# Kernel tuning notes

Hardware: AMD Instinct MI355X
Metric: run time of the kernel (lower is better)

The kernel has to match this reference:

```python
import jax, jax.numpy as jnp
import numpy as np

NEG_SLOPE = 0.2

def gat_conv(x, src, dst, W, a_src, a_dst, b, n_nodes):
    # x: [N, Fin] -> h: [N, Fout]; edges (src->dst) incl. self-loops
    h = x @ W                                   # [N, Fout]
    as_ = h @ a_src                             # [N] per-node source score
    ad_ = h @ a_dst                             # [N] per-node dest score
    e = jax.nn.leaky_relu(as_[src] + ad_[dst], NEG_SLOPE)   # [E]
    # segment softmax over edges sharing the same destination
    e_max = jax.ops.segment_max(e, dst, num_segments=n_nodes)
    e_exp = jnp.exp(e - e_max[dst])
    e_sum = jax.ops.segment_sum(e_exp, dst, num_segments=n_nodes)
    alpha = e_exp / (e_sum[dst] + 1e-16)        # [E]
    out = jax.ops.segment_sum(alpha[:, None] * h[src], dst, num_segments=n_nodes)
    return out + b

def setup_inputs() -> dict:
    key = jax.random.key(0)
    ks = jax.random.split(key, 12)
    N, E, Fin, H = 100000, 3200000, 128, 32
    def g(k, shape, scale):
        return jax.random.normal(k, shape, dtype=jnp.float32) * scale
    return {
        "x": g(ks[0], (N, Fin), 1.0),
        "edge_index": jax.random.randint(ks[1], (2, E), 0, N, dtype=jnp.int32),
        "W1": g(ks[2], (Fin, H), 1.0 / np.sqrt(Fin)),
        "att_src1": g(ks[3], (H,), 1.0 / np.sqrt(H)),
        "att_dst1": g(ks[4], (H,), 1.0 / np.sqrt(H)),
        "b1": jnp.zeros((H,), jnp.float32),
        "W2": g(ks[5], (H, H), 1.0 / np.sqrt(H)),
        "att_src2": g(ks[6], (H,), 1.0 / np.sqrt(H)),
        "att_dst2": g(ks[7], (H,), 1.0 / np.sqrt(H)),
        "b2": jnp.zeros((H,), jnp.float32),
        "Wf": g(ks[8], (H, H), 1.0 / np.sqrt(H)),
        "bf": jnp.zeros((H,), jnp.float32),
    }

def reference(x, edge_index, W1, att_src1, att_dst1, b1, W2, att_src2, att_dst2, b2, Wf, bf):
    n_nodes = x.shape[0]
    loops = jnp.arange(n_nodes, dtype=edge_index.dtype)
    src = jnp.concatenate([edge_index[0], loops])  # add_self_loops=True (PyG default)
    dst = jnp.concatenate([edge_index[1], loops])
    h = jax.nn.relu(gat_conv(x, src, dst, W1, att_src1, att_dst1, b1, n_nodes))
    h = jax.nn.relu(gat_conv(h, src, dst, W2, att_src2, att_dst2, b2, n_nodes))
    return h @ Wf + bf
```

## Files before the change

### kernel.cpp

```cpp
#include <hip/hip_runtime.h>

#define NEG_SLOPE 0.2f
#define BK_SH 8
#define BK_SZ 256
#define MAXBUCK 512
#define EPB 8192

typedef _Float16 half8 __attribute__((ext_vector_type(8)));
typedef float f32x4 __attribute__((ext_vector_type(4)));

__global__ __launch_bounds__(256) void k_castx(const float* __restrict__ x,
                                               _Float16* __restrict__ xh,
                                               int n8) {
  int i = blockIdx.x * 256 + threadIdx.x;
  if (i >= n8) return;
  const float4* p = reinterpret_cast<const float4*>(x) + 2 * (size_t)i;
  float4 v0 = p[0], v1 = p[1];
  half8 h;
  h[0] = (_Float16)v0.x; h[1] = (_Float16)v0.y;
  h[2] = (_Float16)v0.z; h[3] = (_Float16)v0.w;
  h[4] = (_Float16)v1.x; h[5] = (_Float16)v1.y;
  h[6] = (_Float16)v1.z; h[7] = (_Float16)v1.w;
  *(reinterpret_cast<half8*>(xh) + i) = h;
}

__global__ __launch_bounds__(256) void k_castW(const float* __restrict__ W,
                                               _Float16* __restrict__ Wt) {
  for (int i = threadIdx.x; i < 128 * 32; i += 256) {
    int k = i >> 5, f = i & 31;
    Wt[f * 128 + k] = (_Float16)W[i];
  }
}

__global__ __launch_bounds__(256) void k_feat_mfma(
    const _Float16* __restrict__ xh, const _Float16* __restrict__ Wt,
    const float* __restrict__ a_src, const float* __restrict__ a_dst,
    _Float16* __restrict__ Hh, float* __restrict__ as_, float* __restrict__ ad_,
    int N) {
  int w = threadIdx.x >> 6;
  int lane = threadIdx.x & 63;
  int base = (blockIdx.x * 4 + w) * 16;
  if (base >= N) return;
  int row16 = lane & 15;
  int kg = lane >> 4;
  f32x4 acc0 = {0.f, 0.f, 0.f, 0.f};
  f32x4 acc1 = {0.f, 0.f, 0.f, 0.f};
  const half8* xa =
      reinterpret_cast<const half8*>(xh + (size_t)(base + row16) * 128 + kg * 8);
#pragma unroll
  for (int kt = 0; kt < 4; ++kt) {
    half8 a = xa[kt * 4];
    half8 b0 = *reinterpret_cast<const half8*>(Wt + (size_t)row16 * 128 +
                                               kt * 32 + kg * 8);
    half8 b1 = *reinterpret_cast<const half8*>(Wt + (size_t)(16 + row16) * 128 +
                                               kt * 32 + kg * 8);
    acc0 = __builtin_amdgcn_mfma_f32_16x16x32_f16(a, b0, acc0, 0, 0, 0);
    acc1 = __builtin_amdgcn_mfma_f32_16x16x32_f16(a, b1, acc1, 0, 0, 0);
  }
  float aS0 = a_src[row16], aS1 = a_src[16 + row16];
  float aD0 = a_dst[row16], aD1 = a_dst[16 + row16];
  float tS[4], tD[4];
#pragma unroll
  for (int r = 0; r < 4; ++r) {
    int row = base + kg * 4 + r;
    Hh[(size_t)row * 32 + row16] = (_Float16)acc0[r];
    Hh[(size_t)row * 32 + 16 + row16] = (_Float16)acc1[r];
    tS[r] = acc0[r] * aS0 + acc1[r] * aS1;
    tD[r] = acc0[r] * aD0 + acc1[r] * aD1;
  }
#pragma unroll
  for (int off = 1; off <= 8; off <<= 1) {
#pragma unroll
    for (int r = 0; r < 4; ++r) {
      tS[r] += __shfl_xor(tS[r], off, 64);
      tD[r] += __shfl_xor(tD[r], off, 64);
    }
  }
  if (row16 == 0) {
#pragma unroll
    for (int r = 0; r < 4; ++r) {
      as_[base + kg * 4 + r] = tS[r];
      ad_[base + kg * 4 + r] = tD[r];
    }
  }
}

__global__ __launch_bounds__(256) void k_feat32(
    const float* __restrict__ X, const float* __restrict__ W,
    const float* __restrict__ a_src, const float* __restrict__ a_dst,
    _Float16* __restrict__ Hh, float* __restrict__ as_, float* __restrict__ ad_,
    int N) {
  __shared__ float sW[32 * 32];
  __shared__ float sX[8][32];
  for (int i = threadIdx.x; i < 32 * 32; i += 256) sW[i] = W[i];
  int node0 = blockIdx.x * 8;
  {
    int i = threadIdx.x;
    int n = node0 + (i >> 5);
    sX[i >> 5][i & 31] = (n < N) ? X[(size_t)n * 32 + (i & 31)] : 0.f;
  }
  __syncthreads();
  int g = threadIdx.x >> 5;
  int f = threadIdx.x & 31;
  int n = node0 + g;
  if (n >= N) return;
  float acc = 0.f;
#pragma unroll
  for (int k = 0; k < 32; ++k) acc += sX[g][k] * sW[k * 32 + f];
  Hh[(size_t)n * 32 + f] = (_Float16)acc;
  float vs = acc * a_src[f];
  float vd = acc * a_dst[f];
#pragma unroll
  for (int off = 16; off; off >>= 1) {
    vs += __shfl_down(vs, off, 32);
    vd += __shfl_down(vd, off, 32);
  }
  if (f == 0) {
    as_[n] = vs;
    ad_[n] = vd;
  }
}

__global__ __launch_bounds__(256) void k_zero(int* __restrict__ p, int n) {
  int i = blockIdx.x * 256 + threadIdx.x;
  if (i < n) p[i] = 0;
}

__global__ __launch_bounds__(256) void k_bhist(const int* __restrict__ ei,
                                               int E, int* __restrict__ bcnt,
                                               int nbuck) {
  __shared__ int h[MAXBUCK];
  for (int i = threadIdx.x; i < nbuck; i += 256) h[i] = 0;
  __syncthreads();
  long base = (long)blockIdx.x * EPB;
#pragma unroll 4
  for (int i = 0; i < EPB / 256; ++i) {
    long e = base + i * 256 + threadIdx.x;
    if (e < E) atomicAdd(&h[ei[E + e] >> BK_SH], 1);
  }
  __syncthreads();
  for (int i = threadIdx.x; i < nbuck; i += 256)
    if (h[i]) atomicAdd(&bcnt[i], h[i]);
}

__global__ __launch_bounds__(1024) void k_scan(const int* __restrict__ bcnt,
                                               int* __restrict__ boff,
                                               int* __restrict__ bcur,
                                               int* __restrict__ ptr, int nbuck,
                                               int N, int E) {
  __shared__ int s[1024];
  int t = threadIdx.x;
  int v = (t < nbuck) ? bcnt[t] : 0;
  s[t] = v;
  __syncthreads();
  for (int off = 1; off < 1024; off <<= 1) {
    int x = (t >= off) ? s[t - off] : 0;
    __syncthreads();
    s[t] += x;
    __syncthreads();
  }
  if (t < nbuck) {
    boff[t] = s[t] - v;
    bcur[t] = s[t] - v;
  }
  if (t == 0) {
    boff[nbuck] = E;
    ptr[N] = E;
  }
}

__global__ __launch_bounds__(256) void k_binA(const int* __restrict__ ei, int E,
                                              int* __restrict__ bcur,
                                              unsigned* __restrict__ packed,
                                              int nbuck) {
  __shared__ int h[MAXBUCK];
  __shared__ int lbase[MAXBUCK];
  for (int i = threadIdx.x; i < nbuck; i += 256) h[i] = 0;
  __syncthreads();
  long base = (long)blockIdx.x * EPB;
#pragma unroll 4
  for (int i = 0; i < EPB / 256; ++i) {
    long e = base + i * 256 + threadIdx.x;
    if (e < E) atomicAdd(&h[ei[E + e] >> BK_SH], 1);
  }
  __syncthreads();
  for (int i = threadIdx.x; i < nbuck; i += 256) {
    lbase[i] = h[i] ? atomicAdd(&bcur[i], h[i]) : 0;
    h[i] = 0;
  }
  __syncthreads();
#pragma unroll 4
  for (int i = 0; i < EPB / 256; ++i) {
    long e = base + i * 256 + threadIdx.x;
    if (e < E) {
      int s = ei[e], d = ei[E + e];
      int b = d >> BK_SH;
      int slot = atomicAdd(&h[b], 1);
      packed[(size_t)lbase[b] + slot] =
          ((unsigned)s << 8) | (unsigned)(d & (BK_SZ - 1));
    }
  }
}

__global__ __launch_bounds__(256) void k_binB(const unsigned* __restrict__ packed,
                                              const int* __restrict__ boff,
                                              int* __restrict__ ptr,
                                              int* __restrict__ srcs, int N) {
  int b = blockIdx.x;
  int beg = boff[b], end = boff[b + 1];
  int t = threadIdx.x;
  __shared__ int lcnt[BK_SZ];
  __shared__ int sc[BK_SZ];
  __shared__ int lcur[BK_SZ];
  lcnt[t] = 0;
  __syncthreads();
  for (int i = beg + t; i < end; i += 256)
    atomicAdd(&lcnt[packed[i] & (BK_SZ - 1)], 1);
  __syncthreads();
  int v = lcnt[t];
  sc[t] = v;
  __syncthreads();
  for (int off = 1; off < 256; off <<= 1) {
    int x = (t >= off) ? sc[t - off] : 0;
    __syncthreads();
    sc[t] += x;
    __syncthreads();
  }
  int excl = sc[t] - v;
  int node = (b << BK_SH) + t;
  if (node < N) ptr[node] = beg + excl;
  lcur[t] = excl;
  __syncthreads();
  for (int i = beg + t; i < end; i += 256) {
    unsigned p = packed[i];
    int slot = atomicAdd(&lcur[p & (BK_SZ - 1)], 1);
    srcs[(size_t)beg + slot] = (int)(p >> 8);
  }
}

__global__ __launch_bounds__(256) void k_gather(
    const int* __restrict__ ptr, const int* __restrict__ srcs,
    const _Float16* __restrict__ Hh, const float* __restrict__ as_,
    const float* __restrict__ ad_, const float* __restrict__ b,
    float* __restrict__ OUT, int N, int do_relu) {
  int g = threadIdx.x >> 5;
  int lane = threadIdx.x & 31;
  int sub = lane >> 2;
  int q = lane & 3;
  int d = blockIdx.x * 8 + g;
  if (d >= N) return;
  float ad_d = ad_[d];
  float acc[8] = {0.f, 0.f, 0.f, 0.f, 0.f, 0.f, 0.f, 0.f};
  float sumw = 0.f;
  int beg = ptr[d], end = ptr[d + 1];
  for (int j = beg; j < end; j += 8) {
    if (sub < end - j) {
      int sid = srcs[j + sub];
      float sc2 = as_[sid] + ad_d;
      float el = sc2 > 0.f ? sc2 : NEG_SLOPE * sc2;
      float w = __expf(el);
      half8 hv = *reinterpret_cast<const half8*>(Hh + (size_t)sid * 32 + q * 8);
#pragma unroll
      for (int i = 0; i < 8; ++i) acc[i] += w * (float)hv[i];
      sumw += w;
    }
  }
#pragma unroll
  for (int off = 4; off <= 16; off <<= 1) {
#pragma unroll
    for (int i = 0; i < 8; ++i) acc[i] += __shfl_xor(acc[i], off, 32);
    sumw += __shfl_xor(sumw, off, 32);
  }
  if (sub == 0) {
    float s0 = as_[d] + ad_d;
    float e0 = s0 > 0.f ? s0 : NEG_SLOPE * s0;
    float w0 = __expf(e0);
    half8 hs = *reinterpret_cast<const half8*>(Hh + (size_t)d * 32 + q * 8);
#pragma unroll
    for (int i = 0; i < 8; ++i) acc[i] += w0 * (float)hs[i];
    sumw += w0;
    float inv = 1.f / (sumw + 1e-16f);
    float4 o1, o2;
    o1.x = acc[0] * inv + b[q * 8 + 0];
    o1.y = acc[1] * inv + b[q * 8 + 1];
    o1.z = acc[2] * inv + b[q * 8 + 2];
    o1.w = acc[3] * inv + b[q * 8 + 3];
    o2.x = acc[4] * inv + b[q * 8 + 4];
    o2.y = acc[5] * inv + b[q * 8 + 5];
    o2.z = acc[6] * inv + b[q * 8 + 6];
    o2.w = acc[7] * inv + b[q * 8 + 7];
    if (do_relu) {
      o1.x = fmaxf(o1.x, 0.f); o1.y = fmaxf(o1.y, 0.f);
      o1.z = fmaxf(o1.z, 0.f); o1.w = fmaxf(o1.w, 0.f);
      o2.x = fmaxf(o2.x, 0.f); o2.y = fmaxf(o2.y, 0.f);
      o2.z = fmaxf(o2.z, 0.f); o2.w = fmaxf(o2.w, 0.f);
    }
    *reinterpret_cast<float4*>(OUT + (size_t)d * 32 + q * 8) = o1;
    *reinterpret_cast<float4*>(OUT + (size_t)d * 32 + q * 8 + 4) = o2;
  }
}

__global__ __launch_bounds__(256) void k_final(
    const float* __restrict__ X, const float* __restrict__ W,
    const float* __restrict__ b, float* __restrict__ OUT, int N) {
  __shared__ float sW[32 * 32];
  __shared__ float sX[8][32];
  for (int i = threadIdx.x; i < 32 * 32; i += 256) sW[i] = W[i];
  int node0 = blockIdx.x * 8;
  {
    int i = threadIdx.x;
    int n = node0 + (i >> 5);
    sX[i >> 5][i & 31] = (n < N) ? X[(size_t)n * 32 + (i & 31)] : 0.f;
  }
  __syncthreads();
  int g = threadIdx.x >> 5;
  int f = threadIdx.x & 31;
  int n = node0 + g;
  if (n >= N) return;
  float acc = b[f];
#pragma unroll
  for (int k = 0; k < 32; ++k) acc += sX[g][k] * sW[k * 32 + f];
  OUT[(size_t)n * 32 + f] = acc;
}

extern "C" void kernel_launch(void* const* d_in, const int* in_sizes, int n_in,
                              void* d_out, int out_size, void* d_ws,
                              size_t ws_size, hipStream_t stream) {
  const float* x = (const float*)d_in[0];
  const int* ei = (const int*)d_in[1];
  const float* W1 = (const float*)d_in[2];
  const float* as1 = (const float*)d_in[3];
  const float* ad1 = (const float*)d_in[4];
  const float* b1 = (const float*)d_in[5];
  const float* W2 = (const float*)d_in[6];
  const float* as2 = (const float*)d_in[7];
  const float* ad2 = (const float*)d_in[8];
  const float* b2 = (const float*)d_in[9];
  const float* Wf = (const float*)d_in[10];
  const float* bf = (const float*)d_in[11];
  float* out = (float*)d_out;

  const int H = in_sizes[3];
  const int FIN = in_sizes[2] / H;
  const int N = in_sizes[0] / FIN;
  const int E = in_sizes[1] / 2;
  const int nbuck = (N + BK_SZ - 1) >> BK_SH;
  (void)n_in; (void)out_size; (void)ws_size; (void)H;

  size_t r0 = (size_t)E * 4;
  size_t xhB = (size_t)N * FIN * 2;
  size_t bfB = (size_t)N * 32 * 4;
  if (xhB > r0) r0 = xhB;
  if (bfB > r0) r0 = bfB;
  char* basep = (char*)d_ws;
  unsigned* packed = (unsigned*)basep;
  _Float16* xh = (_Float16*)basep;
  float* Bf = (float*)basep;
  char* p = basep + r0;
  _Float16* Hh = (_Float16*)p;  p += (size_t)N * 32 * 2;
  _Float16* Wt = (_Float16*)p;  p += (size_t)128 * 32 * 2;
  float* asv = (float*)p;       p += (size_t)N * 4;
  float* adv = (float*)p;       p += (size_t)N * 4;
  int* ptr = (int*)p;           p += (size_t)(N + 1) * 4;
  int* srcs = (int*)p;          p += (size_t)E * 4;
  int* bcnt = (int*)p;          p += (size_t)nbuck * 4;
  int* boff = (int*)p;          p += (size_t)(nbuck + 1) * 4;
  int* bcur = (int*)p;

  const int nodeBlocks = (N + 7) / 8;
  const int binBlocks = (E + EPB - 1) / EPB;
  const int mfmaBlocks = (N / 16 + 3) / 4;

  k_zero<<<(nbuck + 255) / 256, 256, 0, stream>>>(bcnt, nbuck);
  k_bhist<<<binBlocks, 256, 0, stream>>>(ei, E, bcnt, nbuck);
  k_scan<<<1, 1024, 0, stream>>>(bcnt, boff, bcur, ptr, nbuck, N, E);
  k_binA<<<binBlocks, 256, 0, stream>>>(ei, E, bcur, packed, nbuck);
  k_binB<<<nbuck, 256, 0, stream>>>(packed, boff, ptr, srcs, N);

  k_castx<<<(N * FIN / 8 + 255) / 256, 256, 0, stream>>>(x, xh, N * FIN / 8);
  k_castW<<<1, 256, 0, stream>>>(W1, Wt);
  k_feat_mfma<<<mfmaBlocks, 256, 0, stream>>>(xh, Wt, as1, ad1, Hh, asv, adv, N);
  k_gather<<<nodeBlocks, 256, 0, stream>>>(ptr, srcs, Hh, asv, adv, b1, Bf, N, 1);

  k_feat32<<<nodeBlocks, 256, 0, stream>>>(Bf, W2, as2, ad2, Hh, asv, adv, N);
  k_gather<<<nodeBlocks, 256, 0, stream>>>(ptr, srcs, Hh, asv, adv, b2, Bf, N, 1);

  k_final<<<nodeBlocks, 256, 0, stream>>>(Bf, Wf, bf, out, N);
}
```

Before: 260.9 us.

## Stage binned edges in shared memory before coalesced scatter to global

The binning kernel now builds a block-local counting sort in LDS. It prefix-sums the bucket histogram, places each record into a shared staging array, and then writes them out to global memory in bucket order. This targets the scattered, uncoalesced global stores of the previous direct per-edge scatter. In exchange it uses about 48KB of LDS per block, which lowers occupancy, and adds a scan with extra barriers.

Measured after the change: 253.1 us. 1.03x faster.

```diff
diff --git a/kernel.cpp b/kernel.cpp
--- a/kernel.cpp
+++ b/kernel.cpp
@@ -175,30 +175,54 @@
                                               int nbuck) {
   __shared__ int h[MAXBUCK];
   __shared__ int lbase[MAXBUCK];
-  for (int i = threadIdx.x; i < nbuck; i += 256) h[i] = 0;
+  __shared__ int lb[MAXBUCK];
+  __shared__ int cur[MAXBUCK];
+  __shared__ int psum[256];
+  __shared__ unsigned rec[EPB];
+  __shared__ unsigned short bkt[EPB];
+  int t = threadIdx.x;
+  for (int i = t; i < MAXBUCK; i += 256) h[i] = 0;
   __syncthreads();
   long base = (long)blockIdx.x * EPB;
+  int cnt = (int)((E - base) < EPB ? (E - base) : EPB);
 #pragma unroll 4
   for (int i = 0; i < EPB / 256; ++i) {
-    long e = base + i * 256 + threadIdx.x;
-    if (e < E) atomicAdd(&h[ei[E + e] >> BK_SH], 1);
-  }
-  __syncthreads();
-  for (int i = threadIdx.x; i < nbuck; i += 256) {
+    int e = i * 256 + t;
+    if (e < cnt) atomicAdd(&h[ei[E + base + e] >> BK_SH], 1);
+  }
+  __syncthreads();
+  for (int i = t; i < nbuck; i += 256)
     lbase[i] = h[i] ? atomicAdd(&bcur[i], h[i]) : 0;
-    h[i] = 0;
-  }
+  int a0 = h[2 * t], a1 = h[2 * t + 1];
+  psum[t] = a0 + a1;
+  __syncthreads();
+  for (int off = 1; off < 256; off <<= 1) {
+    int x = (t >= off) ? psum[t - off] : 0;
+    __syncthreads();
+    psum[t] += x;
+    __syncthreads();
+  }
+  int pex = psum[t] - (a0 + a1);
+  lb[2 * t] = pex;
+  lb[2 * t + 1] = pex + a0;
+  cur[2 * t] = pex;
+  cur[2 * t + 1] = pex + a0;
   __syncthreads();
 #pragma unroll 4
   for (int i = 0; i < EPB / 256; ++i) {
-    long e = base + i * 256 + threadIdx.x;
-    if (e < E) {
-      int s = ei[e], d = ei[E + e];
+    int e = i * 256 + t;
+    if (e < cnt) {
+      int s = ei[base + e], d = ei[E + base + e];
       int b = d >> BK_SH;
-      int slot = atomicAdd(&h[b], 1);
-      packed[(size_t)lbase[b] + slot] =
-          ((unsigned)s << 8) | (unsigned)(d & (BK_SZ - 1));
+      int pos = atomicAdd(&cur[b], 1);
+      rec[pos] = ((unsigned)s << 8) | (unsigned)(d & (BK_SZ - 1));
+      bkt[pos] = (unsigned short)b;
     }
+  }
+  __syncthreads();
+  for (int i = t; i < cnt; i += 256) {
+    int b = bkt[i];
+    packed[(size_t)lbase[b] + (i - lb[b])] = rec[i];
   }
 }
 
```
